# Optimization experiments

Hardware: AMD Instinct MI355X
Metric: run time of the kernel (lower is better)

## Reference

```python
import jax, jax.numpy as jnp
import numpy as np

NEG_INF = -1e30


def _rope_interleaved(x, freqs):
    # x: [B,S,H,D], freqs broadcastable [1,S,1,D]; interleaved even/odd rotation
    x0 = x[..., 0::2]
    x1 = x[..., 1::2]
    f0 = freqs[..., 0::2]
    f1 = freqs[..., 1::2]
    o0 = f0 * x0 - f1 * x1
    o1 = f1 * x0 + f0 * x1
    # interleave back: out[...,0::2]=o0, out[...,1::2]=o1
    out = jnp.stack([o0, o1], axis=-1)  # [B,S,H,D/2,2]
    return out.reshape(x.shape).astype(x.dtype)


def setup_inputs() -> dict:
    key = jax.random.key(0)
    kq, kk, kv, kf = jax.random.split(key, 4)
    B, S, H, D = 2, 2048, 16, 128
    q = jax.random.normal(kq, (B, S, H, D), dtype=jnp.float32)
    k = jax.random.normal(kk, (B, S, H, D), dtype=jnp.float32)
    v = jax.random.normal(kv, (B, S, H, D), dtype=jnp.float32)
    freqs = jax.random.normal(kf, (1, S, 1, D), dtype=jnp.float32)
    return {"q": q, "k": k, "v": v, "freqs": freqs}


def reference(q, k, v, freqs):
    # RoPE (Wan-style indexed interleaved write) on q and k
    rq = _rope_interleaved(q, freqs)  # [B,S,H,D]
    rk = _rope_interleaved(k, freqs)
    B, S, H, D = q.shape
    scale = 1.0 / jnp.sqrt(jnp.asarray(D, dtype=q.dtype))
    # transpose(1,2) -> [B,H,S,D]; fused into einsum subscripts
    scores = jnp.einsum("bqhd,bkhd->bhqk", rq, rk) * scale  # [B,H,S,S]
    causal = jnp.tril(jnp.ones((S, S), dtype=bool))
    scores = jnp.where(causal[None, None, :, :], scores, NEG_INF)
    probs = jax.nn.softmax(scores, axis=-1)
    out = jnp.einsum("bhqk,bkhd->bhqd", probs, v)  # [B,H,S,D]
    return out
```

## Files before the change

### kernel.cpp

```cpp
#include <hip/hip_runtime.h>
#include <hip/hip_bf16.h>

#define B_  2
#define S_  2048
#define H_  16
#define D_  128
#define BQ  128
#define BK  64
#define SH  (H_ * D_)
#define NT  (S_ / 64)
#define NTQ (S_ / BQ)
#define TILE_US 8192

typedef __attribute__((ext_vector_type(8))) short bf16x8;
typedef __attribute__((ext_vector_type(4))) float f32x4;
typedef __attribute__((ext_vector_type(4))) unsigned int u32x4;

__device__ __forceinline__ ushort f2bf(float x) {
  union { float f; unsigned u; } c; c.f = x;
  unsigned u = c.u;
  return (ushort)((u + 0x7FFFu + ((u >> 16) & 1u)) >> 16);
}

__device__ __forceinline__ void gload_lds16(const ushort* g, ushort* l) {
  __builtin_amdgcn_global_load_lds((const __attribute__((address_space(1))) void*)g,
                                   (__attribute__((address_space(3))) void*)l,
                                   16, 0, 0);
}

__device__ __forceinline__ bf16x8 ntload8(const ushort* p) {
  union { u32x4 u; bf16x8 v; } c;
  c.u = __builtin_nontemporal_load((const u32x4*)p);
  return c.v;
}

__global__ __launch_bounds__(256)
void pack_all(const float* __restrict__ qg, const float* __restrict__ kg,
              const float* __restrict__ vg, const float* __restrict__ fg,
              ushort* __restrict__ qr, ushort* __restrict__ kr,
              ushort* __restrict__ vt) {
  __shared__ float sv[64][133];
  const int bhp = blockIdx.x;
  const int t   = blockIdx.y;
  const int b   = bhp >> 4;
  const int h   = bhp & 15;
  const int tid = threadIdx.x;
  const float QS = 0.08838834764831845f * 1.4426950408889634f;
  const size_t tbase = ((size_t)(b * H_ + h) * NT + t) * TILE_US;

  #pragma unroll
  for (int c = 0; c < 4; c++) {
    const int idx = tid + 256 * c;
    const int row = idx >> 4;
    const int cu  = idx & 15;
    const int col = cu * 8;
    const int s   = t * 64 + row;
    const size_t goff = ((size_t)(b * S_ + s)) * SH + (size_t)h * D_ + col;

    const float4 f0 = *(const float4*)(fg + (size_t)s * D_ + col);
    const float4 f1 = *(const float4*)(fg + (size_t)s * D_ + col + 4);
    const float4 qx0 = *(const float4*)(qg + goff);
    const float4 qx1 = *(const float4*)(qg + goff + 4);
    const float4 kx0 = *(const float4*)(kg + goff);
    const float4 kx1 = *(const float4*)(kg + goff + 4);
    const float4 vx0 = *(const float4*)(vg + goff);
    const float4 vx1 = *(const float4*)(vg + goff + 4);

    *(float4*)&sv[row][col]     = vx0;
    *(float4*)&sv[row][col + 4] = vx1;

    union { ushort s[8]; uint4 v; } pq, pk;
    pq.s[0] = f2bf((f0.x*qx0.x - f0.y*qx0.y) * QS);
    pq.s[1] = f2bf((f0.y*qx0.x + f0.x*qx0.y) * QS);
    pq.s[2] = f2bf((f0.z*qx0.z - f0.w*qx0.w) * QS);
    pq.s[3] = f2bf((f0.w*qx0.z + f0.z*qx0.w) * QS);
    pq.s[4] = f2bf((f1.x*qx1.x - f1.y*qx1.y) * QS);
    pq.s[5] = f2bf((f1.y*qx1.x + f1.x*qx1.y) * QS);
    pq.s[6] = f2bf((f1.z*qx1.z - f1.w*qx1.w) * QS);
    pq.s[7] = f2bf((f1.w*qx1.z + f1.z*qx1.w) * QS);
    pk.s[0] = f2bf(f0.x*kx0.x - f0.y*kx0.y);
    pk.s[1] = f2bf(f0.y*kx0.x + f0.x*kx0.y);
    pk.s[2] = f2bf(f0.z*kx0.z - f0.w*kx0.w);
    pk.s[3] = f2bf(f0.w*kx0.z + f0.z*kx0.w);
    pk.s[4] = f2bf(f1.x*kx1.x - f1.y*kx1.y);
    pk.s[5] = f2bf(f1.y*kx1.x + f1.x*kx1.y);
    pk.s[6] = f2bf(f1.z*kx1.z - f1.w*kx1.w);
    pk.s[7] = f2bf(f1.w*kx1.z + f1.z*kx1.w);

    const int pos = ((cu >> 2) * 4 + (row >> 4)) * 64 + ((row & 15) | ((cu & 3) << 4));
    *(uint4*)(qr + tbase + (size_t)pos * 8) = pq.v;
    *(uint4*)(kr + tbase + (size_t)pos * 8) = pk.v;
  }
  __syncthreads();

  #pragma unroll
  for (int c = 0; c < 4; c++) {
    const int u2  = tid + 256 * c;
    const int g2  = u2 >> 6;
    const int ln  = u2 & 63;
    const int dim = (g2 & 7) * 16 + (ln & 15);
    const int k0  = (g2 >> 3) * 32 + (ln >> 4) * 8;
    union { ushort s[8]; uint4 v; } p;
    #pragma unroll
    for (int j = 0; j < 8; j++) p.s[j] = f2bf(sv[k0 + j][dim]);
    *(uint4*)(vt + tbase + (size_t)u2 * 8) = p.v;
  }
}

__global__ __launch_bounds__(256, 2)
void fattn4(const ushort* __restrict__ qr, const ushort* __restrict__ kr,
            const ushort* __restrict__ vt, float* __restrict__ og) {
  __shared__ __align__(16) ushort sK[2][TILE_US];
  __shared__ __align__(16) ushort sV[2][TILE_US];
  __shared__ __align__(16) ushort sP[4][2048];

  const int bh_  = blockIdx.x;
  const int y    = (int)blockIdx.y;
  const int qt   = (y & 1) ? (y >> 1) : (NTQ - 1 - (y >> 1));
  const int tid  = threadIdx.x;
  const int wv   = tid >> 6;
  const int lane = tid & 63;
  const int l15  = lane & 15;
  const int quad = lane >> 4;

  const size_t bh = (size_t)bh_;
  const ushort* ktb = kr + bh * NT * TILE_US;
  const ushort* vtb = vt + bh * NT * TILE_US;

  bf16x8 afq[2][4];
  {
    const ushort* qtb64 = qr + (bh * NT + 2 * qt + (wv >> 1)) * TILE_US;
    const int rbb = (wv & 1) * 2;
    #pragma unroll
    for (int rh = 0; rh < 2; rh++)
      #pragma unroll
      for (int ks = 0; ks < 4; ks++)
        afq[rh][ks] = ntload8(qtb64 + (size_t)((ks * 4 + rbb + rh) * 64 + lane) * 8);
  }

  float rs[2][4];
  f32x4 o_acc[2][8];
  #pragma unroll
  for (int rh = 0; rh < 2; rh++) {
    #pragma unroll
    for (int r = 0; r < 4; r++) rs[rh][r] = 0.0f;
    #pragma unroll
    for (int dt = 0; dt < 8; dt++) o_acc[rh][dt] = (f32x4)0.0f;
  }

  #pragma unroll
  for (int c = 0; c < 4; c++) {
    const int g = wv * 4 + c;
    gload_lds16(ktb + g * 512 + lane * 8, &sK[0][g * 512 + lane * 8]);
    gload_lds16(vtb + g * 512 + lane * 8, &sV[0][g * 512 + lane * 8]);
  }

  const int rowmax = qt * BQ + wv * 32 + 31;
  const int nkt = 2 * qt + 2;
  int buf = 0;
  for (int kt = 0; kt < nkt; kt++) {
    __syncthreads();

    if (kt + 1 < nkt) {
      const ushort* ksrc = ktb + (size_t)(kt + 1) * TILE_US;
      const ushort* vsrc = vtb + (size_t)(kt + 1) * TILE_US;
      #pragma unroll
      for (int c = 0; c < 4; c++) {
        const int g = wv * 4 + c;
        gload_lds16(ksrc + g * 512 + lane * 8, &sK[buf ^ 1][g * 512 + lane * 8]);
        gload_lds16(vsrc + g * 512 + lane * 8, &sV[buf ^ 1][g * 512 + lane * 8]);
      }
    }

    if (kt * 64 <= rowmax) {
      f32x4 sc[2][4];
      #pragma unroll
      for (int rh = 0; rh < 2; rh++)
        #pragma unroll
        for (int nt = 0; nt < 4; nt++) sc[rh][nt] = (f32x4)0.0f;
      __builtin_amdgcn_s_setprio(1);
      #pragma unroll
      for (int nt = 0; nt < 4; nt++) {
        #pragma unroll
        for (int ks = 0; ks < 4; ks++) {
          const bf16x8 bk_ = *(const bf16x8*)&sK[buf][(size_t)((ks * 4 + nt) * 64 + lane) * 8];
          sc[0][nt] = __builtin_amdgcn_mfma_f32_16x16x32_bf16(afq[0][ks], bk_, sc[0][nt], 0, 0, 0);
          sc[1][nt] = __builtin_amdgcn_mfma_f32_16x16x32_bf16(afq[1][ks], bk_, sc[1][nt], 0, 0, 0);
        }
      }
      __builtin_amdgcn_s_setprio(0);

      if (kt >= 2 * qt) {
        #pragma unroll
        for (int rh = 0; rh < 2; rh++) {
          #pragma unroll
          for (int nt = 0; nt < 4; nt++) {
            const int col = kt * 64 + nt * 16 + l15;
            #pragma unroll
            for (int r = 0; r < 4; r++) {
              const int row = qt * 128 + wv * 32 + rh * 16 + quad * 4 + r;
              if (col > row) sc[rh][nt][r] = -1e30f;
            }
          }
        }
      }

      #pragma unroll
      for (int rh = 0; rh < 2; rh++) {
        #pragma unroll
        for (int nt = 0; nt < 4; nt++) {
          const int base = rh * 1024 + (nt >> 1) * 512
                         + (((nt & 1) << 1) | (l15 >> 3)) * 128 + (l15 & 7);
          #pragma unroll
          for (int r = 0; r < 4; r++) {
            const float p = __builtin_amdgcn_exp2f(sc[rh][nt][r]);
            rs[rh][r] += p;
            sP[wv][base + (quad * 4 + r) * 8] = f2bf(p);
          }
        }
      }

      bf16x8 ap[2][2];
      #pragma unroll
      for (int rh = 0; rh < 2; rh++)
        #pragma unroll
        for (int ks = 0; ks < 2; ks++)
          ap[rh][ks] = *(const bf16x8*)&sP[wv][(size_t)(rh * 1024 + (ks * 64 + lane) * 8)];
      __builtin_amdgcn_s_setprio(1);
      #pragma unroll
      for (int dt = 0; dt < 8; dt++) {
        #pragma unroll
        for (int ks = 0; ks < 2; ks++) {
          const bf16x8 bv = *(const bf16x8*)&sV[buf][(size_t)((ks * 8 + dt) * 64 + lane) * 8];
          o_acc[0][dt] = __builtin_amdgcn_mfma_f32_16x16x32_bf16(ap[0][ks], bv, o_acc[0][dt], 0, 0, 0);
          o_acc[1][dt] = __builtin_amdgcn_mfma_f32_16x16x32_bf16(ap[1][ks], bv, o_acc[1][dt], 0, 0, 0);
        }
      }
      __builtin_amdgcn_s_setprio(0);
    }

    buf ^= 1;
  }

  float* ob = og + (bh * S_ + (size_t)qt * BQ) * D_;
  #pragma unroll
  for (int rh = 0; rh < 2; rh++) {
    #pragma unroll
    for (int r = 0; r < 4; r++) {
      float t = rs[rh][r];
      t += __shfl_xor(t, 1);
      t += __shfl_xor(t, 2);
      t += __shfl_xor(t, 4);
      t += __shfl_xor(t, 8);
      const float inv = 1.0f / t;
      const int row = wv * 32 + rh * 16 + quad * 4 + r;
      #pragma unroll
      for (int dt = 0; dt < 8; dt++)
        __builtin_nontemporal_store(o_acc[rh][dt][r] * inv,
                                    &ob[(size_t)row * D_ + dt * 16 + l15]);
    }
  }
}

extern "C" void kernel_launch(void* const* d_in, const int* in_sizes, int n_in,
                              void* d_out, int out_size, void* d_ws, size_t ws_size,
                              hipStream_t stream) {
  const float* q = (const float*)d_in[0];
  const float* k = (const float*)d_in[1];
  const float* v = (const float*)d_in[2];
  const float* f = (const float*)d_in[3];
  float* o = (float*)d_out;

  const size_t NELT = (size_t)B_ * S_ * H_ * D_;
  ushort* qr = (ushort*)d_ws;
  ushort* kr = qr + NELT;
  ushort* vt = kr + NELT;

  dim3 block(256);
  pack_all<<<dim3(B_ * H_, NT), block, 0, stream>>>(q, k, v, f, qr, kr, vt);
  fattn4<<<dim3(B_ * H_, NTQ), block, 0, stream>>>(qr, kr, vt, o);
}
```

Before: 205.4 us.

## Compute transposed scores so P stays in registers, removing LDS round-trip

Swaps the MFMA operand order so the QK^T accumulator holds keys along the register dimension, which lets the exponentiated probabilities be packed directly into bf16 A-operands with v_cvt_pk_bf16 instead of being written to and re-read from shared memory. The V tile packing is permuted to match the new key ordering, the row-sum reduction is reworked accordingly, and the sP shared buffer is removed. It also drops the s_setprio hints and replaces the interleaved q-tile ordering with a simple descending order, which may change load balance across the causal workload.

Result: faster. 196.6 us (-4.3%).

```diff
diff --git a/kernel.cpp b/kernel.cpp
--- a/kernel.cpp
+++ b/kernel.cpp
@@ -32,6 +32,12 @@
   union { u32x4 u; bf16x8 v; } c;
   c.u = __builtin_nontemporal_load((const u32x4*)p);
   return c.v;
+}
+
+__device__ __forceinline__ unsigned cvt_pk_bf16(float lo, float hi) {
+  unsigned d;
+  asm("v_cvt_pk_bf16_f32 %0, %1, %2" : "=v"(d) : "v"(lo), "v"(hi));
+  return d;
 }
 
 __global__ __launch_bounds__(256)
@@ -99,10 +105,14 @@
     const int g2  = u2 >> 6;
     const int ln  = u2 & 63;
     const int dim = (g2 & 7) * 16 + (ln & 15);
-    const int k0  = (g2 >> 3) * 32 + (ln >> 4) * 8;
+    const int ks2 = g2 >> 3;
+    const int qd  = ln >> 4;
     union { ushort s[8]; uint4 v; } p;
     #pragma unroll
-    for (int j = 0; j < 8; j++) p.s[j] = f2bf(sv[k0 + j][dim]);
+    for (int j = 0; j < 8; j++) {
+      const int key = ks2 * 32 + (j >> 2) * 16 + qd * 4 + (j & 3);
+      p.s[j] = f2bf(sv[key][dim]);
+    }
     *(uint4*)(vt + tbase + (size_t)u2 * 8) = p.v;
   }
 }
@@ -112,11 +122,9 @@
             const ushort* __restrict__ vt, float* __restrict__ og) {
   __shared__ __align__(16) ushort sK[2][TILE_US];
   __shared__ __align__(16) ushort sV[2][TILE_US];
-  __shared__ __align__(16) ushort sP[4][2048];
 
   const int bh_  = blockIdx.x;
-  const int y    = (int)blockIdx.y;
-  const int qt   = (y & 1) ? (y >> 1) : (NTQ - 1 - (y >> 1));
+  const int qt   = NTQ - 1 - (int)blockIdx.y;
   const int tid  = threadIdx.x;
   const int wv   = tid >> 6;
   const int lane = tid & 63;
@@ -138,15 +146,12 @@
         afq[rh][ks] = ntload8(qtb64 + (size_t)((ks * 4 + rbb + rh) * 64 + lane) * 8);
   }
 
-  float rs[2][4];
+  float rs[2] = {0.0f, 0.0f};
   f32x4 o_acc[2][8];
   #pragma unroll
-  for (int rh = 0; rh < 2; rh++) {
-    #pragma unroll
-    for (int r = 0; r < 4; r++) rs[rh][r] = 0.0f;
+  for (int rh = 0; rh < 2; rh++)
     #pragma unroll
     for (int dt = 0; dt < 8; dt++) o_acc[rh][dt] = (f32x4)0.0f;
-  }
 
   #pragma unroll
   for (int c = 0; c < 4; c++) {
@@ -178,55 +183,53 @@
       for (int rh = 0; rh < 2; rh++)
         #pragma unroll
         for (int nt = 0; nt < 4; nt++) sc[rh][nt] = (f32x4)0.0f;
-      __builtin_amdgcn_s_setprio(1);
       #pragma unroll
       for (int nt = 0; nt < 4; nt++) {
         #pragma unroll
         for (int ks = 0; ks < 4; ks++) {
           const bf16x8 bk_ = *(const bf16x8*)&sK[buf][(size_t)((ks * 4 + nt) * 64 + lane) * 8];
-          sc[0][nt] = __builtin_amdgcn_mfma_f32_16x16x32_bf16(afq[0][ks], bk_, sc[0][nt], 0, 0, 0);
-          sc[1][nt] = __builtin_amdgcn_mfma_f32_16x16x32_bf16(afq[1][ks], bk_, sc[1][nt], 0, 0, 0);
-        }
-      }
-      __builtin_amdgcn_s_setprio(0);
+          sc[0][nt] = __builtin_amdgcn_mfma_f32_16x16x32_bf16(bk_, afq[0][ks], sc[0][nt], 0, 0, 0);
+          sc[1][nt] = __builtin_amdgcn_mfma_f32_16x16x32_bf16(bk_, afq[1][ks], sc[1][nt], 0, 0, 0);
+        }
+      }
 
       if (kt >= 2 * qt) {
         #pragma unroll
         for (int rh = 0; rh < 2; rh++) {
+          const int qg = qt * 128 + wv * 32 + rh * 16 + l15;
           #pragma unroll
           for (int nt = 0; nt < 4; nt++) {
-            const int col = kt * 64 + nt * 16 + l15;
+            const int kg = kt * 64 + nt * 16 + quad * 4;
             #pragma unroll
-            for (int r = 0; r < 4; r++) {
-              const int row = qt * 128 + wv * 32 + rh * 16 + quad * 4 + r;
-              if (col > row) sc[rh][nt][r] = -1e30f;
-            }
+            for (int r = 0; r < 4; r++)
+              if (kg + r > qg) sc[rh][nt][r] = -1e30f;
           }
         }
       }
 
+      bf16x8 ap[2][2];
       #pragma unroll
       for (int rh = 0; rh < 2; rh++) {
-        #pragma unroll
-        for (int nt = 0; nt < 4; nt++) {
-          const int base = rh * 1024 + (nt >> 1) * 512
-                         + (((nt & 1) << 1) | (l15 >> 3)) * 128 + (l15 & 7);
+        float p[4][4];
+        #pragma unroll
+        for (int nt = 0; nt < 4; nt++)
           #pragma unroll
           for (int r = 0; r < 4; r++) {
-            const float p = __builtin_amdgcn_exp2f(sc[rh][nt][r]);
-            rs[rh][r] += p;
-            sP[wv][base + (quad * 4 + r) * 8] = f2bf(p);
+            p[nt][r] = __builtin_amdgcn_exp2f(sc[rh][nt][r]);
+            rs[rh] += p[nt][r];
           }
-        }
-      }
-
-      bf16x8 ap[2][2];
-      #pragma unroll
-      for (int rh = 0; rh < 2; rh++)
-        #pragma unroll
-        for (int ks = 0; ks < 2; ks++)
-          ap[rh][ks] = *(const bf16x8*)&sP[wv][(size_t)(rh * 1024 + (ks * 64 + lane) * 8)];
-      __builtin_amdgcn_s_setprio(1);
+        #pragma unroll
+        for (int ks = 0; ks < 2; ks++) {
+          union { unsigned u[4]; bf16x8 v; } pk_;
+          #pragma unroll
+          for (int m = 0; m < 4; m++) {
+            const int nt = ks * 2 + (m >> 1);
+            pk_.u[m] = cvt_pk_bf16(p[nt][2 * (m & 1)], p[nt][2 * (m & 1) + 1]);
+          }
+          ap[rh][ks] = pk_.v;
+        }
+      }
+
       #pragma unroll
       for (int dt = 0; dt < 8; dt++) {
         #pragma unroll
@@ -236,7 +239,6 @@
           o_acc[1][dt] = __builtin_amdgcn_mfma_f32_16x16x32_bf16(ap[1][ks], bv, o_acc[1][dt], 0, 0, 0);
         }
       }
-      __builtin_amdgcn_s_setprio(0);
     }
 
     buf ^= 1;
@@ -245,14 +247,12 @@
   float* ob = og + (bh * S_ + (size_t)qt * BQ) * D_;
   #pragma unroll
   for (int rh = 0; rh < 2; rh++) {
+    float t = rs[rh];
+    t += __shfl_xor(t, 16);
+    t += __shfl_xor(t, 32);
     #pragma unroll
     for (int r = 0; r < 4; r++) {
-      float t = rs[rh][r];
-      t += __shfl_xor(t, 1);
-      t += __shfl_xor(t, 2);
-      t += __shfl_xor(t, 4);
-      t += __shfl_xor(t, 8);
-      const float inv = 1.0f / t;
+      const float inv = 1.0f / __shfl(t, quad * 4 + r);
       const int row = wv * 32 + rh * 16 + quad * 4 + r;
       #pragma unroll
       for (int dt = 0; dt < 8; dt++)
```
